# Kernel optimization log

Hardware: AMD Instinct MI355X
Metric: run time of the kernel (lower is better)

Reference implementation:

```python
import jax, jax.numpy as jnp
import numpy as np

H = 100          # hidden size (hard-coded in module)
B, C, T = 256, 9, 1024
NC = 6           # num_classes


def _lstm_layer(xs, W_ih, W_hh, b, h0, c0):
    """xs: [B,T,In] -> hidden sequence [B,T,H]. Torch gate order i,f,g,o."""
    # Precompute the input projection for all timesteps in one big GEMM.
    pre = jnp.einsum('bti,gi->btg', xs, W_ih) + b   # [B,T,4H]
    pre_t = jnp.swapaxes(pre, 0, 1)                 # [T,B,4H]

    def step(carry, p):
        h, c = carry
        g = p + h @ W_hh.T                          # [B,4H]
        i, f, gg, o = jnp.split(g, 4, axis=-1)
        c = jax.nn.sigmoid(f) * c + jax.nn.sigmoid(i) * jnp.tanh(gg)
        h = jax.nn.sigmoid(o) * jnp.tanh(c)
        return (h, c), h

    (_, _), hs = jax.lax.scan(step, (h0, c0), pre_t)
    return jnp.swapaxes(hs, 0, 1)                   # [B,T,H]


def setup_inputs() -> dict:
    key = jax.random.key(0)
    ks = jax.random.split(key, 14)
    s = 0.1  # ~ uniform(-1/sqrt(H), 1/sqrt(H)) scale of torch default init
    n = lambda k, shape, sc=s: jax.random.normal(k, shape, dtype=jnp.float32) * sc
    return {
        'x':     jax.random.normal(ks[0], (B, C, T), dtype=jnp.float32),
        'h0_1':  jax.random.normal(ks[1], (B, H), dtype=jnp.float32),
        'c0_1':  jax.random.normal(ks[2], (B, H), dtype=jnp.float32),
        'h0_2':  jax.random.normal(ks[3], (B, H), dtype=jnp.float32),
        'c0_2':  jax.random.normal(ks[4], (B, H), dtype=jnp.float32),
        'W_ih1': n(ks[5], (4 * H, C)),
        'W_hh1': n(ks[6], (4 * H, H)),
        'b1':    n(ks[7], (4 * H,)),   # b_ih + b_hh folded together
        'W_ih2': n(ks[8], (4 * H, H)),
        'W_hh2': n(ks[9], (4 * H, H)),
        'b2':    n(ks[10], (4 * H,)),
        'W_fc':  n(ks[11], (NC, H)),
        'b_fc':  n(ks[12], (NC,)),
    }


def reference(x, h0_1, c0_1, h0_2, c0_2, W_ih1, W_hh1, b1,
              W_ih2, W_hh2, b2, W_fc, b_fc):
    xs = jnp.swapaxes(x, 1, 2)                      # [B,T,C] (x.transpose(1,2))
    h1 = _lstm_layer(xs, W_ih1, W_hh1, b1, h0_1, c0_1)   # [B,T,H]
    h2 = _lstm_layer(h1, W_ih2, W_hh2, b2, h0_2, c0_2)   # [B,T,H]
    out = h2[:, -1, :] @ W_fc.T + b_fc              # [B,NC]
    return out
```

## Files before the change

### kernel.cpp

```cpp
#include <hip/hip_runtime.h>

#define HH   100
#define G4   400
#define BB   256
#define CC   9
#define TT   1024
#define NCLS 6
#define XSTR 13

__device__ __forceinline__ float sigm(float x) {
    return __fdividef(1.0f, 1.0f + __expf(-x));
}
__device__ __forceinline__ float tanh_fast(float x) {
    return 2.0f * sigm(2.0f * x) - 1.0f;
}
__device__ __forceinline__ float bcast(float v, int l) {
    return __int_as_float(__builtin_amdgcn_readlane(__float_as_int(v), l));
}

__global__ __launch_bounds__(896, 2)
void lstm_layer1(const float* __restrict__ x,
                 const float* __restrict__ h0,
                 const float* __restrict__ c0,
                 const float* __restrict__ W_ih,
                 const float* __restrict__ W_hh,
                 const float* __restrict__ bias_g,
                 float* __restrict__ h1out)
{
    const int b    = blockIdx.x;
    const int tid  = threadIdx.x;
    const int lane = tid & 63;

    __shared__ float xT[TT * XSTR + 64];
    __shared__ float hb[128];
    __shared__ float p[2][448];

    const float* xb = x + (size_t)b * CC * TT;
    for (int i = tid; i < CC * TT; i += 896) {
        int c  = i >> 10;
        int tp = i & 1023;
        xT[tp * XSTR + c] = xb[i];
    }
    if (tid < 128) hb[tid] = (tid < HH) ? h0[b * HH + tid] : 0.0f;
    float c_reg = (tid < HH) ? c0[b * HH + tid] : 0.0f;

    const bool half0 = (tid < 448);
    const int  r     = half0 ? tid : (tid - 448);
    const int  row   = (r < G4) ? r : 0;

    float w[55], bg = 0.0f;
    if (half0) {
        #pragma unroll
        for (int j = 0; j < CC; ++j) w[j] = W_ih[row * CC + j];
        #pragma unroll
        for (int j = 0; j < 46; ++j) w[CC + j] = W_hh[row * HH + j];
        bg = bias_g[row];
    } else {
        #pragma unroll
        for (int j = 0; j < 54; ++j) w[j] = W_hh[row * HH + 46 + j];
        w[54] = 0.0f;
    }
    #pragma unroll
    for (int j = 0; j < 55; ++j) asm volatile("" : "+v"(w[j]));

    float* hout = h1out + (size_t)b * TT * HH;
    __syncthreads();

    for (int t = 0; t < TT; ++t) {
        if (half0) {
            float vx = xT[t * XSTR + lane];
            float va = hb[lane];
            asm volatile("" : "+v"(vx), "+v"(va));
            float a0 = bg, a1 = 0.f;
            #pragma unroll
            for (int c = 0; c < CC; ++c) {
                float h_ = bcast(vx, c);
                if (c & 1) a1 += h_ * w[c]; else a0 += h_ * w[c];
            }
            #pragma unroll
            for (int j = 0; j < 46; ++j) {
                float h_ = bcast(va, j);
                if (j & 1) a1 += h_ * w[CC + j]; else a0 += h_ * w[CC + j];
            }
            p[0][tid] = a0 + a1;
        } else {
            float vb = hb[46 + lane];
            asm volatile("" : "+v"(vb));
            float a0 = 0.f, a1 = 0.f;
            #pragma unroll
            for (int j = 0; j < 54; ++j) {
                float h_ = bcast(vb, j);
                if (j & 1) a1 += h_ * w[j]; else a0 += h_ * w[j];
            }
            p[1][tid - 448] = a0 + a1;
        }
        __syncthreads();
        if (tid < HH) {
            float ri = p[0][tid]          + p[1][tid];
            float rf = p[0][tid + HH]     + p[1][tid + HH];
            float rg = p[0][tid + 2 * HH] + p[1][tid + 2 * HH];
            float ro = p[0][tid + 3 * HH] + p[1][tid + 3 * HH];
            float cc = sigm(rf) * c_reg + sigm(ri) * tanh_fast(rg);
            c_reg = cc;
            float hv = sigm(ro) * tanh_fast(cc);
            hb[tid] = hv;
            hout[t * HH + tid] = hv;
        }
        __syncthreads();
    }
}

__global__ __launch_bounds__(960, 2)
void lstm_layer2_fc(const float* __restrict__ h1,
                    const float* __restrict__ h0,
                    const float* __restrict__ c0,
                    const float* __restrict__ W_ih,
                    const float* __restrict__ W_hh,
                    const float* __restrict__ bias_g,
                    const float* __restrict__ W_fc,
                    const float* __restrict__ b_fc,
                    float* __restrict__ out)
{
    const int b    = blockIdx.x;
    const int tid  = threadIdx.x;
    const int lane = tid & 63;

    __shared__ float h1buf[2][128];
    __shared__ float h2b[128];
    __shared__ float p[2][448];

    if (tid < 128) {
        h2b[tid] = (tid < HH) ? h0[b * HH + tid] : 0.0f;
        h1buf[0][tid] = 0.0f;
        h1buf[1][tid] = 0.0f;
    }
    float c_reg = (tid < HH) ? c0[b * HH + tid] : 0.0f;

    const bool comp  = (tid < 896);
    const bool half0 = (tid < 448);
    const int  r     = half0 ? tid : (tid - 448);
    const int  row   = (r < G4) ? r : 0;

    float w[HH], bg = 0.0f;
    {
        const float* wsrc = half0 ? (W_ih + row * HH) : (W_hh + row * HH);
        #pragma unroll
        for (int j = 0; j < HH; ++j) w[j] = wsrc[j];
        if (half0) bg = bias_g[row];
    }
    #pragma unroll
    for (int j = 0; j < HH; ++j) asm volatile("" : "+v"(w[j]));

    const float* h1b = h1 + (size_t)b * TT * HH;
    __syncthreads();

    if (tid >= 896) {
        int i = tid - 896;
        if (i < HH / 4)
            ((float4*)h1buf[0])[i] = ((const float4*)h1b)[i];
    }
    __syncthreads();

    for (int t = 0; t < TT; ++t) {
        const int cur = t & 1;
        if (comp) {
            const float* hsrc = half0 ? h1buf[cur] : h2b;
            float va = hsrc[lane];
            float vb = hsrc[64 + lane];
            asm volatile("" : "+v"(va), "+v"(vb));
            float a0 = bg, a1 = 0.f;
            #pragma unroll
            for (int j = 0; j < 64; ++j) {
                float h_ = bcast(va, j);
                if (j & 1) a1 += h_ * w[j]; else a0 += h_ * w[j];
            }
            #pragma unroll
            for (int j = 0; j < 36; ++j) {
                float h_ = bcast(vb, j);
                if (j & 1) a1 += h_ * w[64 + j]; else a0 += h_ * w[64 + j];
            }
            p[half0 ? 0 : 1][r] = a0 + a1;
        } else if ((t + 1) < TT) {
            int i = tid - 896;
            if (i < HH / 4)
                ((float4*)h1buf[cur ^ 1])[i] =
                    ((const float4*)(h1b + (t + 1) * HH))[i];
        }
        __syncthreads();
        if (tid < HH) {
            float ri = p[0][tid]          + p[1][tid];
            float rf = p[0][tid + HH]     + p[1][tid + HH];
            float rg = p[0][tid + 2 * HH] + p[1][tid + 2 * HH];
            float ro = p[0][tid + 3 * HH] + p[1][tid + 3 * HH];
            float cc = sigm(rf) * c_reg + sigm(ri) * tanh_fast(rg);
            c_reg = cc;
            h2b[tid] = sigm(ro) * tanh_fast(cc);
        }
        __syncthreads();
    }

    if (tid < NCLS) {
        float acc = b_fc[tid];
        #pragma unroll 4
        for (int j = 0; j < HH; ++j) acc += W_fc[tid * HH + j] * h2b[j];
        out[b * NCLS + tid] = acc;
    }
}

extern "C" void kernel_launch(void* const* d_in, const int* in_sizes, int n_in,
                              void* d_out, int out_size, void* d_ws, size_t ws_size,
                              hipStream_t stream) {
    const float* x     = (const float*)d_in[0];
    const float* h0_1  = (const float*)d_in[1];
    const float* c0_1  = (const float*)d_in[2];
    const float* h0_2  = (const float*)d_in[3];
    const float* c0_2  = (const float*)d_in[4];
    const float* W_ih1 = (const float*)d_in[5];
    const float* W_hh1 = (const float*)d_in[6];
    const float* b1    = (const float*)d_in[7];
    const float* W_ih2 = (const float*)d_in[8];
    const float* W_hh2 = (const float*)d_in[9];
    const float* b2    = (const float*)d_in[10];
    const float* W_fc  = (const float*)d_in[11];
    const float* b_fc  = (const float*)d_in[12];
    float* out = (float*)d_out;

    float* h1 = (float*)d_ws;

    lstm_layer1<<<BB, 896, 0, stream>>>(x, h0_1, c0_1, W_ih1, W_hh1, b1, h1);
    lstm_layer2_fc<<<BB, 960, 0, stream>>>(h1, h0_2, c0_2, W_ih2, W_hh2, b2,
                                           W_fc, b_fc, out);
}
```

Measured before the change: 2.500 ms.

## Chunk timesteps, precompute input projections per chunk, split gate dot-products across quarters

Both LSTM kernels now process time in chunks of 64 steps. For each chunk they first compute the input projection for every step and store it in a shared-memory buffer, which takes it off the serial recurrence path. The recurrent matvec is remapped so each of 512 threads owns one hidden unit and one quarter of the K range for all four gates. Partial sums are combined with LDS atomicAdd, and the biases are added in the elementwise update. This shortens per-step work and drops the per-step h1 prefetch. In exchange it adds atomic contention, chunk-level zeroing and syncs, and a large shared-memory footprint.

```diff
diff --git a/kernel.cpp b/kernel.cpp
--- a/kernel.cpp
+++ b/kernel.cpp
@@ -6,7 +6,11 @@
 #define CC   9
 #define TT   1024
 #define NCLS 6
-#define XSTR 13
+#define CH   64
+#define NCH  (TT/CH)
+#define HT_STR 144
+#define HB_PAD 144
+#define XT_STR 16
 
 __device__ __forceinline__ float sigm(float x) {
     return __fdividef(1.0f, 1.0f + __expf(-x));
@@ -18,105 +22,135 @@
     return __int_as_float(__builtin_amdgcn_readlane(__float_as_int(v), l));
 }
 
-__global__ __launch_bounds__(896, 2)
+__global__ __launch_bounds__(512) __attribute__((amdgpu_waves_per_eu(2, 2)))
 void lstm_layer1(const float* __restrict__ x,
                  const float* __restrict__ h0,
                  const float* __restrict__ c0,
                  const float* __restrict__ W_ih,
                  const float* __restrict__ W_hh,
-                 const float* __restrict__ bias_g,
+                 const float* __restrict__ bias,
                  float* __restrict__ h1out)
 {
     const int b    = blockIdx.x;
     const int tid  = threadIdx.x;
     const int lane = tid & 63;
-
-    __shared__ float xT[TT * XSTR + 64];
-    __shared__ float hb[128];
-    __shared__ float p[2][448];
-
-    const float* xb = x + (size_t)b * CC * TT;
-    for (int i = tid; i < CC * TT; i += 896) {
-        int c  = i >> 10;
-        int tp = i & 1023;
-        xT[tp * XSTR + c] = xb[i];
-    }
-    if (tid < 128) hb[tid] = (tid < HH) ? h0[b * HH + tid] : 0.0f;
-    float c_reg = (tid < HH) ? c0[b * HH + tid] : 0.0f;
-
-    const bool half0 = (tid < 448);
-    const int  r     = half0 ? tid : (tid - 448);
-    const int  row   = (r < G4) ? r : 0;
-
-    float w[55], bg = 0.0f;
-    if (half0) {
-        #pragma unroll
-        for (int j = 0; j < CC; ++j) w[j] = W_ih[row * CC + j];
-        #pragma unroll
-        for (int j = 0; j < 46; ++j) w[CC + j] = W_hh[row * HH + j];
-        bg = bias_g[row];
+    const int q    = tid >> 7;
+    const int u    = tid & 127;
+    const int uc   = (u < HH) ? u : 0;
+
+    __shared__ float xt[CH * XT_STR + 80];
+    __shared__ float preS[CH * G4];
+    __shared__ float hb[HB_PAD];
+
+    float whh[4][25];
+    #pragma unroll
+    for (int g = 0; g < 4; ++g) {
+        const float* src = W_hh + (size_t)(g * HH + uc) * HH + q * 25;
+        #pragma unroll
+        for (int e = 0; e < 25; ++e) whh[g][e] = src[e];
+    }
+    float wx[4][3];
+    if (q < 3) {
+        #pragma unroll
+        for (int g = 0; g < 4; ++g) {
+            const float* s = W_ih + (size_t)(g * HH + uc) * CC + q * 3;
+            #pragma unroll
+            for (int e = 0; e < 3; ++e) wx[g][e] = s[e];
+        }
     } else {
         #pragma unroll
-        for (int j = 0; j < 54; ++j) w[j] = W_hh[row * HH + 46 + j];
-        w[54] = 0.0f;
-    }
-    #pragma unroll
-    for (int j = 0; j < 55; ++j) asm volatile("" : "+v"(w[j]));
-
-    float* hout = h1out + (size_t)b * TT * HH;
-    __syncthreads();
-
-    for (int t = 0; t < TT; ++t) {
-        if (half0) {
-            float vx = xT[t * XSTR + lane];
-            float va = hb[lane];
-            asm volatile("" : "+v"(vx), "+v"(va));
-            float a0 = bg, a1 = 0.f;
-            #pragma unroll
-            for (int c = 0; c < CC; ++c) {
-                float h_ = bcast(vx, c);
-                if (c & 1) a1 += h_ * w[c]; else a0 += h_ * w[c];
-            }
-            #pragma unroll
-            for (int j = 0; j < 46; ++j) {
-                float h_ = bcast(va, j);
-                if (j & 1) a1 += h_ * w[CC + j]; else a0 += h_ * w[CC + j];
-            }
-            p[0][tid] = a0 + a1;
-        } else {
-            float vb = hb[46 + lane];
-            asm volatile("" : "+v"(vb));
-            float a0 = 0.f, a1 = 0.f;
-            #pragma unroll
-            for (int j = 0; j < 54; ++j) {
-                float h_ = bcast(vb, j);
-                if (j & 1) a1 += h_ * w[j]; else a0 += h_ * w[j];
-            }
-            p[1][tid - 448] = a0 + a1;
-        }
-        __syncthreads();
-        if (tid < HH) {
-            float ri = p[0][tid]          + p[1][tid];
-            float rf = p[0][tid + HH]     + p[1][tid + HH];
-            float rg = p[0][tid + 2 * HH] + p[1][tid + 2 * HH];
-            float ro = p[0][tid + 3 * HH] + p[1][tid + 3 * HH];
-            float cc = sigm(rf) * c_reg + sigm(ri) * tanh_fast(rg);
-            c_reg = cc;
-            float hv = sigm(ro) * tanh_fast(cc);
-            hb[tid] = hv;
-            hout[t * HH + tid] = hv;
-        }
-        __syncthreads();
-    }
-}
-
-__global__ __launch_bounds__(960, 2)
+        for (int g = 0; g < 4; ++g)
+            #pragma unroll
+            for (int e = 0; e < 3; ++e) wx[g][e] = 0.0f;
+    }
+    #pragma unroll
+    for (int g = 0; g < 4; ++g)
+        #pragma unroll
+        for (int e = 0; e < 25; ++e) asm volatile("" : "+v"(whh[g][e]));
+
+    float c_reg = 0.f, bq0 = 0.f, bq1 = 0.f, bq2 = 0.f, bq3 = 0.f;
+    if (tid < HH) {
+        c_reg = c0[b * HH + tid];
+        bq0 = bias[tid];          bq1 = bias[HH + tid];
+        bq2 = bias[2 * HH + tid]; bq3 = bias[3 * HH + tid];
+    }
+    if (tid < HB_PAD) hb[tid] = (tid < HH) ? h0[b * HH + tid] : 0.0f;
+
+    const float* xb   = x + (size_t)b * CC * TT;
+    float*       hout = h1out + (size_t)b * TT * HH;
+
+    for (int ch = 0; ch < NCH; ++ch) {
+        const int t0 = ch * CH;
+        for (int i = tid; i < CH * G4 / 4; i += 512)
+            ((float4*)preS)[i] = make_float4(0.f, 0.f, 0.f, 0.f);
+        for (int i = tid; i < CC * CH; i += 512) {
+            int c  = i >> 6;
+            int ti = i & 63;
+            xt[ti * XT_STR + c] = xb[c * TT + t0 + ti];
+        }
+        __syncthreads();
+
+        if (q < 3) {
+            for (int t = 0; t < CH; ++t) {
+                float vx = xt[t * XT_STR + q * 3 + lane];
+                asm volatile("" : "+v"(vx));
+                float a0 = 0.f, a1 = 0.f, a2 = 0.f, a3 = 0.f;
+                #pragma unroll
+                for (int e = 0; e < 3; ++e) {
+                    float s = bcast(vx, e);
+                    a0 += s * wx[0][e]; a1 += s * wx[1][e];
+                    a2 += s * wx[2][e]; a3 += s * wx[3][e];
+                }
+                if (u < HH) {
+                    atomicAdd(&preS[t * G4 + u],            a0);
+                    atomicAdd(&preS[t * G4 + HH + u],       a1);
+                    atomicAdd(&preS[t * G4 + 2 * HH + u],   a2);
+                    atomicAdd(&preS[t * G4 + 3 * HH + u],   a3);
+                }
+            }
+        }
+        __syncthreads();
+
+        for (int t = 0; t < CH; ++t) {
+            float va = hb[q * 25 + lane];
+            asm volatile("" : "+v"(va));
+            float a0 = 0.f, a1 = 0.f, a2 = 0.f, a3 = 0.f;
+            #pragma unroll
+            for (int e = 0; e < 25; ++e) {
+                float s = bcast(va, e);
+                a0 += s * whh[0][e]; a1 += s * whh[1][e];
+                a2 += s * whh[2][e]; a3 += s * whh[3][e];
+            }
+            if (u < HH) {
+                atomicAdd(&preS[t * G4 + u],            a0);
+                atomicAdd(&preS[t * G4 + HH + u],       a1);
+                atomicAdd(&preS[t * G4 + 2 * HH + u],   a2);
+                atomicAdd(&preS[t * G4 + 3 * HH + u],   a3);
+            }
+            __syncthreads();
+            if (tid < HH) {
+                float ri = preS[t * G4 + tid]          + bq0;
+                float rf = preS[t * G4 + HH + tid]     + bq1;
+                float rg = preS[t * G4 + 2 * HH + tid] + bq2;
+                float ro = preS[t * G4 + 3 * HH + tid] + bq3;
+                float cc2 = sigm(rf) * c_reg + sigm(ri) * tanh_fast(rg);
+                c_reg = cc2;
+                float hv = sigm(ro) * tanh_fast(cc2);
+                hb[tid] = hv;
+                hout[(size_t)(t0 + t) * HH + tid] = hv;
+            }
+            __syncthreads();
+        }
+    }
+}
+
+__global__ __launch_bounds__(512) __attribute__((amdgpu_waves_per_eu(2, 2)))
 void lstm_layer2_fc(const float* __restrict__ h1,
                     const float* __restrict__ h0,
                     const float* __restrict__ c0,
                     const float* __restrict__ W_ih,
                     const float* __restrict__ W_hh,
-                    const float* __restrict__ bias_g,
+                    const float* __restrict__ bias,
                     const float* __restrict__ W_fc,
                     const float* __restrict__ b_fc,
                     float* __restrict__ out)
@@ -124,85 +158,103 @@
     const int b    = blockIdx.x;
     const int tid  = threadIdx.x;
     const int lane = tid & 63;
-
-    __shared__ float h1buf[2][128];
-    __shared__ float h2b[128];
-    __shared__ float p[2][448];
-
-    if (tid < 128) {
-        h2b[tid] = (tid < HH) ? h0[b * HH + tid] : 0.0f;
-        h1buf[0][tid] = 0.0f;
-        h1buf[1][tid] = 0.0f;
-    }
-    float c_reg = (tid < HH) ? c0[b * HH + tid] : 0.0f;
-
-    const bool comp  = (tid < 896);
-    const bool half0 = (tid < 448);
-    const int  r     = half0 ? tid : (tid - 448);
-    const int  row   = (r < G4) ? r : 0;
-
-    float w[HH], bg = 0.0f;
-    {
-        const float* wsrc = half0 ? (W_ih + row * HH) : (W_hh + row * HH);
-        #pragma unroll
-        for (int j = 0; j < HH; ++j) w[j] = wsrc[j];
-        if (half0) bg = bias_g[row];
-    }
-    #pragma unroll
-    for (int j = 0; j < HH; ++j) asm volatile("" : "+v"(w[j]));
-
-    const float* h1b = h1 + (size_t)b * TT * HH;
-    __syncthreads();
-
-    if (tid >= 896) {
-        int i = tid - 896;
-        if (i < HH / 4)
-            ((float4*)h1buf[0])[i] = ((const float4*)h1b)[i];
-    }
-    __syncthreads();
-
-    for (int t = 0; t < TT; ++t) {
-        const int cur = t & 1;
-        if (comp) {
-            const float* hsrc = half0 ? h1buf[cur] : h2b;
-            float va = hsrc[lane];
-            float vb = hsrc[64 + lane];
-            asm volatile("" : "+v"(va), "+v"(vb));
-            float a0 = bg, a1 = 0.f;
-            #pragma unroll
-            for (int j = 0; j < 64; ++j) {
-                float h_ = bcast(va, j);
-                if (j & 1) a1 += h_ * w[j]; else a0 += h_ * w[j];
-            }
-            #pragma unroll
-            for (int j = 0; j < 36; ++j) {
-                float h_ = bcast(vb, j);
-                if (j & 1) a1 += h_ * w[64 + j]; else a0 += h_ * w[64 + j];
-            }
-            p[half0 ? 0 : 1][r] = a0 + a1;
-        } else if ((t + 1) < TT) {
-            int i = tid - 896;
-            if (i < HH / 4)
-                ((float4*)h1buf[cur ^ 1])[i] =
-                    ((const float4*)(h1b + (t + 1) * HH))[i];
-        }
-        __syncthreads();
-        if (tid < HH) {
-            float ri = p[0][tid]          + p[1][tid];
-            float rf = p[0][tid + HH]     + p[1][tid + HH];
-            float rg = p[0][tid + 2 * HH] + p[1][tid + 2 * HH];
-            float ro = p[0][tid + 3 * HH] + p[1][tid + 3 * HH];
-            float cc = sigm(rf) * c_reg + sigm(ri) * tanh_fast(rg);
-            c_reg = cc;
-            h2b[tid] = sigm(ro) * tanh_fast(cc);
-        }
-        __syncthreads();
+    const int q    = tid >> 7;
+    const int u    = tid & 127;
+    const int uc   = (u < HH) ? u : 0;
+
+    __shared__ float h1tile[CH * HT_STR];
+    __shared__ float preS[CH * G4];
+    __shared__ float hb[HB_PAD];
+
+    float wih[4][25], whh[4][25];
+    #pragma unroll
+    for (int g = 0; g < 4; ++g) {
+        const float* si = W_ih + (size_t)(g * HH + uc) * HH + q * 25;
+        const float* sh = W_hh + (size_t)(g * HH + uc) * HH + q * 25;
+        #pragma unroll
+        for (int e = 0; e < 25; ++e) { wih[g][e] = si[e]; whh[g][e] = sh[e]; }
+    }
+    #pragma unroll
+    for (int g = 0; g < 4; ++g)
+        #pragma unroll
+        for (int e = 0; e < 25; ++e)
+            asm volatile("" : "+v"(wih[g][e]), "+v"(whh[g][e]));
+
+    float c_reg = 0.f, bq0 = 0.f, bq1 = 0.f, bq2 = 0.f, bq3 = 0.f;
+    if (tid < HH) {
+        c_reg = c0[b * HH + tid];
+        bq0 = bias[tid];          bq1 = bias[HH + tid];
+        bq2 = bias[2 * HH + tid]; bq3 = bias[3 * HH + tid];
+    }
+    if (tid < HB_PAD) hb[tid] = (tid < HH) ? h0[b * HH + tid] : 0.0f;
+
+    const float* h1g = h1 + (size_t)b * TT * HH;
+
+    for (int ch = 0; ch < NCH; ++ch) {
+        const int t0 = ch * CH;
+        for (int i = tid; i < CH * G4 / 4; i += 512)
+            ((float4*)preS)[i] = make_float4(0.f, 0.f, 0.f, 0.f);
+        for (int i = tid; i < CH * 25; i += 512) {
+            int r  = i / 25;
+            int j4 = i - r * 25;
+            ((float4*)(h1tile + r * HT_STR))[j4] =
+                ((const float4*)(h1g + (size_t)(t0 + r) * HH))[j4];
+        }
+        __syncthreads();
+
+        for (int t = 0; t < CH; ++t) {
+            float va = h1tile[t * HT_STR + q * 25 + lane];
+            asm volatile("" : "+v"(va));
+            float a0 = 0.f, a1 = 0.f, a2 = 0.f, a3 = 0.f;
+            #pragma unroll
+            for (int e = 0; e < 25; ++e) {
+                float s = bcast(va, e);
+                a0 += s * wih[0][e]; a1 += s * wih[1][e];
+                a2 += s * wih[2][e]; a3 += s * wih[3][e];
+            }
+            if (u < HH) {
+                atomicAdd(&preS[t * G4 + u],            a0);
+                atomicAdd(&preS[t * G4 + HH + u],       a1);
+                atomicAdd(&preS[t * G4 + 2 * HH + u],   a2);
+                atomicAdd(&preS[t * G4 + 3 * HH + u],   a3);
+            }
+        }
+        __syncthreads();
+
+        for (int t = 0; t < CH; ++t) {
+            float va = hb[q * 25 + lane];
+            asm volatile("" : "+v"(va));
+            float a0 = 0.f, a1 = 0.f, a2 = 0.f, a3 = 0.f;
+            #pragma unroll
+            for (int e = 0; e < 25; ++e) {
+                float s = bcast(va, e);
+                a0 += s * whh[0][e]; a1 += s * whh[1][e];
+                a2 += s * whh[2][e]; a3 += s * whh[3][e];
+            }
+            if (u < HH) {
+                atomicAdd(&preS[t * G4 + u],            a0);
+                atomicAdd(&preS[t * G4 + HH + u],       a1);
+                atomicAdd(&preS[t * G4 + 2 * HH + u],   a2);
+                atomicAdd(&preS[t * G4 + 3 * HH + u],   a3);
+            }
+            __syncthreads();
+            if (tid < HH) {
+                float ri = preS[t * G4 + tid]          + bq0;
+                float rf = preS[t * G4 + HH + tid]     + bq1;
+                float rg = preS[t * G4 + 2 * HH + tid] + bq2;
+                float ro = preS[t * G4 + 3 * HH + tid] + bq3;
+                float cc2 = sigm(rf) * c_reg + sigm(ri) * tanh_fast(rg);
+                c_reg = cc2;
+                hb[tid] = sigm(ro) * tanh_fast(cc2);
+            }
+            __syncthreads();
+        }
     }
 
     if (tid < NCLS) {
         float acc = b_fc[tid];
         #pragma unroll 4
-        for (int j = 0; j < HH; ++j) acc += W_fc[tid * HH + j] * h2b[j];
+        for (int j = 0; j < HH; ++j) acc += W_fc[tid * HH + j] * hb[j];
         out[b * NCLS + tid] = acc;
     }
 }
@@ -227,7 +279,7 @@
 
     float* h1 = (float*)d_ws;
 
-    lstm_layer1<<<BB, 896, 0, stream>>>(x, h0_1, c0_1, W_ih1, W_hh1, b1, h1);
-    lstm_layer2_fc<<<BB, 960, 0, stream>>>(h1, h0_2, c0_2, W_ih2, W_hh2, b2,
+    lstm_layer1<<<BB, 512, 0, stream>>>(x, h0_1, c0_1, W_ih1, W_hh1, b1, h1);
+    lstm_layer2_fc<<<BB, 512, 0, stream>>>(h1, h0_2, c0_2, W_ih2, W_hh2, b2,
                                            W_fc, b_fc, out);
 }
```

After: 9.052 ms. 3.62x slower.
